# Kernel tuning notes

Measured on AMD Instinct MI355X. Metric: run time of the kernel, lower is better.

## Reference

```python
import jax, jax.numpy as jnp
import numpy as np

T, D, FF, E, K = 512, 2048, 768, 128, 8


def setup_inputs() -> dict:
    key = jax.random.key(0)
    k0, k1, k2, k3, k4 = jax.random.split(key, 5)
    scale = 0.02
    return {
        "hidden_states": jax.random.normal(k0, (T, D), dtype=jnp.float32),
        "w_gate": jax.random.normal(k1, (D, E), dtype=jnp.float32) * scale,  # router
        "w_gate_proj": jax.random.normal(k2, (E, D, FF), dtype=jnp.float32) * scale,
        "w_up_proj": jax.random.normal(k3, (E, D, FF), dtype=jnp.float32) * scale,
        "w_down_proj": jax.random.normal(k4, (E, FF, D), dtype=jnp.float32) * scale,
    }


def reference(hidden_states, w_gate, w_gate_proj, w_up_proj, w_down_proj):
    x = hidden_states  # [T, D]
    # Router: linear -> softmax (fp32) -> top-k -> renormalize (norm_topk_prob=True)
    router_logits = jnp.dot(x, w_gate)  # [T, E]
    probs = jax.nn.softmax(router_logits.astype(jnp.float32), axis=-1)
    topk_w, topk_idx = jax.lax.top_k(probs, K)  # [T, K]
    topk_w = topk_w / jnp.sum(topk_w, axis=-1, keepdims=True)
    topk_w = topk_w.astype(x.dtype)
    # Scatter per-(token,expert) combine weights: [T, E]
    rows = jnp.arange(T)[:, None]
    combine = jnp.zeros((T, E), dtype=x.dtype).at[rows, topk_idx].add(topk_w)
    # Grouped SwiGLU experts: scan over experts, weighted accumulation.
    def body(acc, per_expert):
        wg, wu, wd, s = per_expert  # [D,FF], [D,FF], [FF,D], [T]
        h = jax.nn.silu(jnp.dot(x, wg)) * jnp.dot(x, wu)  # [T, FF]
        return acc + s[:, None] * jnp.dot(h, wd), None

    init = jnp.zeros_like(x)
    out, _ = jax.lax.scan(
        body, init, (w_gate_proj, w_up_proj, w_down_proj, combine.T)
    )
    return out  # [T, D]
```

## Files before the change

### kernel.cpp

```cpp
#include <hip/hip_runtime.h>
#include <hip/hip_bf16.h>

#define TT 512
#define DH 2048
#define FFD 768
#define NE 128
#define TOPK 8
#define CAP 512
#define SMAX 64

typedef __attribute__((ext_vector_type(4))) float f32x4;
typedef __attribute__((ext_vector_type(8))) short short8;

typedef __attribute__((address_space(3))) unsigned int lds_u32_t;
typedef __attribute__((address_space(1))) unsigned int glob_u32_t;

__device__ __forceinline__ short f2bf(float f) {
    __hip_bfloat16 h = __float2bfloat16(f);
    return *reinterpret_cast<short*>(&h);
}

__device__ __forceinline__ void glds16(const float* g, float* l) {
    __builtin_amdgcn_global_load_lds((glob_u32_t*)g, (lds_u32_t*)l, 16, 0, 0);
}

#define VMCNT(N) asm volatile("s_waitcnt vmcnt(" #N ")" ::: "memory")

__global__ __launch_bounds__(256) void moe_init(int* __restrict__ cnt, float4* __restrict__ out)
{
    const int i = blockIdx.x * 256 + threadIdx.x;
    if (i < NE) cnt[i] = 0;
    out[i] = make_float4(0.f, 0.f, 0.f, 0.f);
}

__global__ __launch_bounds__(128) void moe_router(
    const float* __restrict__ x, const float* __restrict__ wg,
    int* __restrict__ cnt, int* __restrict__ tok_list, float* __restrict__ w_list)
{
    const int t = blockIdx.x;
    const int e = threadIdx.x;
    __shared__ float xs[DH];
    __shared__ float red[NE];
    __shared__ int   redi[NE];
    __shared__ float selw[TOPK];
    __shared__ int   seli[TOPK];

    for (int i = e; i < DH; i += 128) xs[i] = x[(size_t)t * DH + i];
    __syncthreads();

    float acc = 0.f;
    #pragma unroll 4
    for (int d = 0; d < DH; ++d)
        acc = fmaf(xs[d], wg[(size_t)d * NE + e], acc);

    red[e] = acc; __syncthreads();
    for (int s = 64; s > 0; s >>= 1) {
        if (e < s) red[e] = fmaxf(red[e], red[e + s]);
        __syncthreads();
    }
    const float mx = red[0];
    __syncthreads();

    float myp = __expf(acc - mx);

    for (int k = 0; k < TOPK; ++k) {
        red[e] = myp; redi[e] = e;
        __syncthreads();
        for (int s = 64; s > 0; s >>= 1) {
            if (e < s) {
                const float v2 = red[e + s]; const int i2 = redi[e + s];
                if (v2 > red[e] || (v2 == red[e] && i2 < redi[e])) { red[e] = v2; redi[e] = i2; }
            }
            __syncthreads();
        }
        if (e == 0) { selw[k] = red[0]; seli[k] = redi[0]; }
        __syncthreads();
        if (e == seli[k]) myp = -1.f;
        __syncthreads();
    }

    if (e == 0) {
        float s8 = 0.f;
        #pragma unroll
        for (int k = 0; k < TOPK; ++k) s8 += selw[k];
        const float inv = 1.f / s8;
        #pragma unroll
        for (int k = 0; k < TOPK; ++k) {
            const int ex = seli[k];
            const float wv = selw[k] * inv;
            const int pos = atomicAdd(&cnt[ex], 1);
            if (pos < CAP) {
                tok_list[ex * CAP + pos] = t * TOPK + k;
                w_list[ex * CAP + pos] = wv;
            }
        }
    }
}

__global__ __launch_bounds__(256) void moe_gather(
    const float* __restrict__ x, const int* __restrict__ cnt,
    const int* __restrict__ tok_list, short* __restrict__ xgb)
{
    const int e = blockIdx.x;
    int n = cnt[e]; if (n > SMAX) n = SMAX;
    const int k = threadIdx.x * 8;
    short* dste = xgb + (size_t)e * SMAX * DH;
    for (int s = 0; s < SMAX; ++s) {
        short8 o = {0, 0, 0, 0, 0, 0, 0, 0};
        if (s < n) {
            const float* xr = x + (size_t)(tok_list[e * CAP + s] >> 3) * DH + k;
            const float4 v0 = *(const float4*)(xr);
            const float4 v1 = *(const float4*)(xr + 4);
            o[0] = f2bf(v0.x); o[1] = f2bf(v0.y); o[2] = f2bf(v0.z); o[3] = f2bf(v0.w);
            o[4] = f2bf(v1.x); o[5] = f2bf(v1.y); o[6] = f2bf(v1.z); o[7] = f2bf(v1.w);
        }
        *(short8*)(dste + (size_t)s * DH + k) = o;
    }
}

__global__ __launch_bounds__(64) void moe_gateup(
    const short* __restrict__ xgb,
    const float* __restrict__ wgp, const float* __restrict__ wup,
    short* __restrict__ hc)
{
    __shared__ __align__(16) float Bsh[2 * 2 * 2048];

    const int e = blockIdx.y;
    const int lane = threadIdx.x;
    const int fl = lane & 15;
    const int g16 = lane >> 4;
    const int koff = g16 * 8;
    const int f0 = blockIdx.x * 64;
    const int lrow = lane >> 4;
    const int lcol = (lane & 15) * 4;

    const short* xge = xgb + (size_t)e * SMAX * DH;
    const float* wgs = wgp + (size_t)e * DH * FFD + f0;
    const float* wus = wup + (size_t)e * DH * FFD + f0;

    f32x4 accg[4][4] = {};
    f32x4 accu[4][4] = {};
    short8 aA[4], aB[4];

    auto ISSUE = [&](int kk, int b) {
        #pragma unroll
        for (int g = 0; g < 8; ++g) {
            const size_t ro = (size_t)(kk + g * 4 + lrow) * FFD + lcol;
            glds16(wgs + ro, &Bsh[b * 2048 + g * 256]);
            glds16(wus + ro, &Bsh[4096 + b * 2048 + g * 256]);
        }
    };
    auto LOADA = [&](int kk, short8 (&a)[4]) {
        #pragma unroll
        for (int fm = 0; fm < 4; ++fm)
            a[fm] = *(const short8*)(xge + (size_t)(fm * 16 + fl) * DH + kk + koff);
    };
    auto COMP = [&](int b, const short8 (&a)[4]) {
        #pragma unroll
        for (int nf = 0; nf < 4; ++nf) {
            const float* bg = &Bsh[b * 2048 + koff * 64 + nf * 16 + fl];
            const float* bu = &Bsh[4096 + b * 2048 + koff * 64 + nf * 16 + fl];
            short8 bfg, bfu;
            #pragma unroll
            for (int j = 0; j < 8; ++j) { bfg[j] = f2bf(bg[j * 64]); bfu[j] = f2bf(bu[j * 64]); }
            #pragma unroll
            for (int fm = 0; fm < 4; ++fm) {
                accg[nf][fm] = __builtin_amdgcn_mfma_f32_16x16x32_bf16(a[fm], bfg, accg[nf][fm], 0, 0, 0);
                accu[nf][fm] = __builtin_amdgcn_mfma_f32_16x16x32_bf16(a[fm], bfu, accu[nf][fm], 0, 0, 0);
            }
        }
    };

    ISSUE(0, 0);
    LOADA(0, aA);
    for (int t = 0; t < 63; ++t) {
        const int kk = (t + 1) * 32;
        ISSUE(kk, (t + 1) & 1);
        if (t & 1) LOADA(kk, aA); else LOADA(kk, aB);
        VMCNT(20);
        if (t & 1) COMP(1, aB); else COMP(0, aA);
    }
    VMCNT(0);
    COMP(1, aB);

    short* hce = hc + (size_t)e * SMAX * FFD + f0;
    #pragma unroll
    for (int nf = 0; nf < 4; ++nf) {
        #pragma unroll
        for (int fm = 0; fm < 4; ++fm) {
            #pragma unroll
            for (int r = 0; r < 4; ++r) {
                const int s = fm * 16 + g16 * 4 + r;
                const float g = accg[nf][fm][r];
                const float u = accu[nf][fm][r];
                const float hv = (g / (1.f + __expf(-g))) * u;
                hce[(size_t)s * FFD + nf * 16 + fl] = f2bf(hv);
            }
        }
    }
}

__global__ __launch_bounds__(64) void moe_down(
    const short* __restrict__ hc, const float* __restrict__ wdp,
    const int* __restrict__ cnt, const int* __restrict__ tok_list,
    const float* __restrict__ w_list, float* __restrict__ out)
{
    __shared__ __align__(16) float Bsh[2 * 2048];

    const int e = blockIdx.y;
    int n = cnt[e]; if (n > SMAX) n = SMAX;
    if (n == 0) return;

    const int lane = threadIdx.x;
    const int fl = lane & 15;
    const int g16 = lane >> 4;
    const int koff = g16 * 8;
    const int d0 = blockIdx.x * 64;
    const int lrow = lane >> 4;
    const int lcol = (lane & 15) * 4;

    const short* hce = hc + (size_t)e * SMAX * FFD;
    const float* wds = wdp + (size_t)e * FFD * DH + d0;

    f32x4 acc[4][4] = {};
    short8 aA[4], aB[4];

    auto ISSUE = [&](int kk, int b) {
        #pragma unroll
        for (int g = 0; g < 8; ++g) {
            const size_t ro = (size_t)(kk + g * 4 + lrow) * DH + lcol;
            glds16(wds + ro, &Bsh[b * 2048 + g * 256]);
        }
    };
    auto LOADA = [&](int kk, short8 (&a)[4]) {
        #pragma unroll
        for (int fm = 0; fm < 4; ++fm)
            a[fm] = *(const short8*)(hce + (size_t)(fm * 16 + fl) * FFD + kk + koff);
    };
    auto COMP = [&](int b, const short8 (&a)[4]) {
        #pragma unroll
        for (int nf = 0; nf < 4; ++nf) {
            const float* bp = &Bsh[b * 2048 + koff * 64 + nf * 16 + fl];
            short8 bf;
            #pragma unroll
            for (int j = 0; j < 8; ++j) bf[j] = f2bf(bp[j * 64]);
            #pragma unroll
            for (int fm = 0; fm < 4; ++fm)
                acc[nf][fm] = __builtin_amdgcn_mfma_f32_16x16x32_bf16(a[fm], bf, acc[nf][fm], 0, 0, 0);
        }
    };

    ISSUE(0, 0);
    LOADA(0, aA);
    for (int t = 0; t < 23; ++t) {
        const int kk = (t + 1) * 32;
        ISSUE(kk, (t + 1) & 1);
        if (t & 1) LOADA(kk, aA); else LOADA(kk, aB);
        VMCNT(12);
        if (t & 1) COMP(1, aB); else COMP(0, aA);
    }
    VMCNT(0);
    COMP(1, aB);

    #pragma unroll
    for (int nf = 0; nf < 4; ++nf) {
        #pragma unroll
        for (int fm = 0; fm < 4; ++fm) {
            #pragma unroll
            for (int r = 0; r < 4; ++r) {
                const int s = fm * 16 + g16 * 4 + r;
                if (s < n) {
                    const int t = tok_list[e * CAP + s] >> 3;
                    const float wt = w_list[e * CAP + s];
                    atomicAdd(out + (size_t)t * DH + d0 + nf * 16 + fl, acc[nf][fm][r] * wt);
                }
            }
        }
    }
}

extern "C" void kernel_launch(void* const* d_in, const int* in_sizes, int n_in,
                              void* d_out, int out_size, void* d_ws, size_t ws_size,
                              hipStream_t stream) {
    const float* x   = (const float*)d_in[0];
    const float* wg  = (const float*)d_in[1];
    const float* wgp = (const float*)d_in[2];
    const float* wup = (const float*)d_in[3];
    const float* wdp = (const float*)d_in[4];
    float* out = (float*)d_out;

    char* ws = (char*)d_ws;
    int*   cnt      = (int*)ws;
    int*   tok_list = (int*)(ws + 1024);
    float* w_list   = (float*)(ws + 1024 + NE * CAP * 4);
    short* xgb      = (short*)(ws + (1 << 20));
    short* hc       = (short*)(ws + (1 << 20) + (size_t)NE * SMAX * DH * 2);

    moe_init<<<1024, 256, 0, stream>>>(cnt, (float4*)out);
    moe_router<<<TT, 128, 0, stream>>>(x, wg, cnt, tok_list, w_list);
    moe_gather<<<NE, 256, 0, stream>>>(x, cnt, tok_list, xgb);
    moe_gateup<<<dim3(FFD / 64, NE), 64, 0, stream>>>(xgb, wgp, wup, hc);
    moe_down<<<dim3(DH / 64, NE), 64, 0, stream>>>(hc, wdp, cnt, tok_list, w_list, out);
}
```

Measured before the change: 813.8 us.

## Triple-buffer weight and activation prefetch in expert GEMMs; fold output zeroing into router

Both the gate/up and down expert kernels move from a double-buffered to a triple-buffered K-loop. Weight tiles stream into three LDS slots and activation fragments into three register sets, with two stages kept in flight and vmcnt waits sized to match. This should hide more global-memory latency while streaming the large fp32 expert weights. In exchange, LDS use per block rises (48 KB in gate/up), which may lower occupancy. Separately, zeroing of the output moves from the init kernel into the router kernel, leaving a tiny init that only clears the expert counters.

```diff
diff --git a/kernel.cpp b/kernel.cpp
--- a/kernel.cpp
+++ b/kernel.cpp
@@ -24,18 +24,20 @@
     __builtin_amdgcn_global_load_lds((glob_u32_t*)g, (lds_u32_t*)l, 16, 0, 0);
 }
 
-#define VMCNT(N) asm volatile("s_waitcnt vmcnt(" #N ")" ::: "memory")
-
-__global__ __launch_bounds__(256) void moe_init(int* __restrict__ cnt, float4* __restrict__ out)
-{
-    const int i = blockIdx.x * 256 + threadIdx.x;
-    if (i < NE) cnt[i] = 0;
-    out[i] = make_float4(0.f, 0.f, 0.f, 0.f);
+template<int N>
+__device__ __forceinline__ void vmwait() {
+    asm volatile("s_waitcnt vmcnt(%0)" :: "i"(N) : "memory");
+}
+
+__global__ __launch_bounds__(128) void moe_init(int* __restrict__ cnt)
+{
+    cnt[threadIdx.x] = 0;
 }
 
 __global__ __launch_bounds__(128) void moe_router(
     const float* __restrict__ x, const float* __restrict__ wg,
-    int* __restrict__ cnt, int* __restrict__ tok_list, float* __restrict__ w_list)
+    int* __restrict__ cnt, int* __restrict__ tok_list, float* __restrict__ w_list,
+    float* __restrict__ out)
 {
     const int t = blockIdx.x;
     const int e = threadIdx.x;
@@ -44,6 +46,11 @@
     __shared__ int   redi[NE];
     __shared__ float selw[TOPK];
     __shared__ int   seli[TOPK];
+
+    float4* outrow = (float4*)(out + (size_t)t * DH);
+    const float4 z4 = make_float4(0.f, 0.f, 0.f, 0.f);
+    #pragma unroll
+    for (int i = 0; i < 4; ++i) outrow[e + i * 128] = z4;
 
     for (int i = e; i < DH; i += 128) xs[i] = x[(size_t)t * DH + i];
     __syncthreads();
@@ -123,7 +130,7 @@
     const float* __restrict__ wgp, const float* __restrict__ wup,
     short* __restrict__ hc)
 {
-    __shared__ __align__(16) float Bsh[2 * 2 * 2048];
+    __shared__ __align__(16) float Bsh[6 * 2048];
 
     const int e = blockIdx.y;
     const int lane = threadIdx.x;
@@ -140,29 +147,36 @@
 
     f32x4 accg[4][4] = {};
     f32x4 accu[4][4] = {};
-    short8 aA[4], aB[4];
-
-    auto ISSUE = [&](int kk, int b) {
+    short8 A0[4], A1[4], A2[4];
+
+    auto ISSUE = [&](int t, int buf) {
+        const int kk = t * 32;
+        float* bg = &Bsh[buf * 2048];
+        float* bu = &Bsh[6144 + buf * 2048];
         #pragma unroll
         for (int g = 0; g < 8; ++g) {
             const size_t ro = (size_t)(kk + g * 4 + lrow) * FFD + lcol;
-            glds16(wgs + ro, &Bsh[b * 2048 + g * 256]);
-            glds16(wus + ro, &Bsh[4096 + b * 2048 + g * 256]);
-        }
-    };
-    auto LOADA = [&](int kk, short8 (&a)[4]) {
+            glds16(wgs + ro, bg + g * 256);
+            glds16(wus + ro, bu + g * 256);
+        }
+    };
+    auto LOADA = [&](int t, short8 (&a)[4]) {
+        const int kk = t * 32 + koff;
         #pragma unroll
         for (int fm = 0; fm < 4; ++fm)
-            a[fm] = *(const short8*)(xge + (size_t)(fm * 16 + fl) * DH + kk + koff);
-    };
-    auto COMP = [&](int b, const short8 (&a)[4]) {
+            a[fm] = *(const short8*)(xge + (size_t)(fm * 16 + fl) * DH + kk);
+    };
+    auto COMP = [&](int buf, const short8 (&a)[4]) {
+        const float* bg = &Bsh[buf * 2048 + koff * 64 + fl];
+        const float* bu = &Bsh[6144 + buf * 2048 + koff * 64 + fl];
         #pragma unroll
         for (int nf = 0; nf < 4; ++nf) {
-            const float* bg = &Bsh[b * 2048 + koff * 64 + nf * 16 + fl];
-            const float* bu = &Bsh[4096 + b * 2048 + koff * 64 + nf * 16 + fl];
             short8 bfg, bfu;
             #pragma unroll
-            for (int j = 0; j < 8; ++j) { bfg[j] = f2bf(bg[j * 64]); bfu[j] = f2bf(bu[j * 64]); }
+            for (int j = 0; j < 8; ++j) {
+                bfg[j] = f2bf(bg[nf * 16 + j * 64]);
+                bfu[j] = f2bf(bu[nf * 16 + j * 64]);
+            }
             #pragma unroll
             for (int fm = 0; fm < 4; ++fm) {
                 accg[nf][fm] = __builtin_amdgcn_mfma_f32_16x16x32_bf16(a[fm], bfg, accg[nf][fm], 0, 0, 0);
@@ -171,17 +185,18 @@
         }
     };
 
-    ISSUE(0, 0);
-    LOADA(0, aA);
-    for (int t = 0; t < 63; ++t) {
-        const int kk = (t + 1) * 32;
-        ISSUE(kk, (t + 1) & 1);
-        if (t & 1) LOADA(kk, aA); else LOADA(kk, aB);
-        VMCNT(20);
-        if (t & 1) COMP(1, aB); else COMP(0, aA);
-    }
-    VMCNT(0);
-    COMP(1, aB);
+    LOADA(0, A0); ISSUE(0, 0);
+    LOADA(1, A1); ISSUE(1, 1);
+    for (int i = 0; i < 20; ++i) {
+        const int t = 3 * i;
+        LOADA(t + 2, A2); ISSUE(t + 2, 2); vmwait<40>(); COMP(0, A0);
+        LOADA(t + 3, A0); ISSUE(t + 3, 0); vmwait<40>(); COMP(1, A1);
+        LOADA(t + 4, A1); ISSUE(t + 4, 1); vmwait<40>(); COMP(2, A2);
+    }
+    LOADA(62, A2); ISSUE(62, 2); vmwait<40>(); COMP(0, A0);
+    LOADA(63, A0); ISSUE(63, 0); vmwait<40>(); COMP(1, A1);
+    vmwait<20>(); COMP(2, A2);
+    vmwait<0>();  COMP(0, A0);
 
     short* hce = hc + (size_t)e * SMAX * FFD + f0;
     #pragma unroll
@@ -205,7 +220,7 @@
     const int* __restrict__ cnt, const int* __restrict__ tok_list,
     const float* __restrict__ w_list, float* __restrict__ out)
 {
-    __shared__ __align__(16) float Bsh[2 * 2048];
+    __shared__ __align__(16) float Bsh[3 * 2048];
 
     const int e = blockIdx.y;
     int n = cnt[e]; if (n > SMAX) n = SMAX;
@@ -223,44 +238,50 @@
     const float* wds = wdp + (size_t)e * FFD * DH + d0;
 
     f32x4 acc[4][4] = {};
-    short8 aA[4], aB[4];
-
-    auto ISSUE = [&](int kk, int b) {
+    short8 A0[4], A1[4], A2[4];
+
+    auto ISSUE = [&](int t, int buf) {
+        const int kk = t * 32;
+        float* bd = &Bsh[buf * 2048];
         #pragma unroll
         for (int g = 0; g < 8; ++g) {
             const size_t ro = (size_t)(kk + g * 4 + lrow) * DH + lcol;
-            glds16(wds + ro, &Bsh[b * 2048 + g * 256]);
-        }
-    };
-    auto LOADA = [&](int kk, short8 (&a)[4]) {
+            glds16(wds + ro, bd + g * 256);
+        }
+    };
+    auto LOADA = [&](int t, short8 (&a)[4]) {
+        const int kk = t * 32 + koff;
         #pragma unroll
         for (int fm = 0; fm < 4; ++fm)
-            a[fm] = *(const short8*)(hce + (size_t)(fm * 16 + fl) * FFD + kk + koff);
-    };
-    auto COMP = [&](int b, const short8 (&a)[4]) {
+            a[fm] = *(const short8*)(hce + (size_t)(fm * 16 + fl) * FFD + kk);
+    };
+    auto COMP = [&](int buf, const short8 (&a)[4]) {
+        const float* bp = &Bsh[buf * 2048 + koff * 64 + fl];
         #pragma unroll
         for (int nf = 0; nf < 4; ++nf) {
-            const float* bp = &Bsh[b * 2048 + koff * 64 + nf * 16 + fl];
             short8 bf;
             #pragma unroll
-            for (int j = 0; j < 8; ++j) bf[j] = f2bf(bp[j * 64]);
+            for (int j = 0; j < 8; ++j) bf[j] = f2bf(bp[nf * 16 + j * 64]);
             #pragma unroll
             for (int fm = 0; fm < 4; ++fm)
                 acc[nf][fm] = __builtin_amdgcn_mfma_f32_16x16x32_bf16(a[fm], bf, acc[nf][fm], 0, 0, 0);
         }
     };
 
-    ISSUE(0, 0);
-    LOADA(0, aA);
-    for (int t = 0; t < 23; ++t) {
-        const int kk = (t + 1) * 32;
-        ISSUE(kk, (t + 1) & 1);
-        if (t & 1) LOADA(kk, aA); else LOADA(kk, aB);
-        VMCNT(12);
-        if (t & 1) COMP(1, aB); else COMP(0, aA);
-    }
-    VMCNT(0);
-    COMP(1, aB);
+    LOADA(0, A0); ISSUE(0, 0);
+    LOADA(1, A1); ISSUE(1, 1);
+    for (int i = 0; i < 6; ++i) {
+        const int t = 3 * i;
+        LOADA(t + 2, A2); ISSUE(t + 2, 2); vmwait<24>(); COMP(0, A0);
+        LOADA(t + 3, A0); ISSUE(t + 3, 0); vmwait<24>(); COMP(1, A1);
+        LOADA(t + 4, A1); ISSUE(t + 4, 1); vmwait<24>(); COMP(2, A2);
+    }
+    LOADA(20, A2); ISSUE(20, 2); vmwait<24>(); COMP(0, A0);
+    LOADA(21, A0); ISSUE(21, 0); vmwait<24>(); COMP(1, A1);
+    LOADA(22, A1); ISSUE(22, 1); vmwait<24>(); COMP(2, A2);
+    LOADA(23, A2); ISSUE(23, 2); vmwait<24>(); COMP(0, A0);
+    vmwait<12>(); COMP(1, A1);
+    vmwait<0>();  COMP(2, A2);
 
     #pragma unroll
     for (int nf = 0; nf < 4; ++nf) {
@@ -296,8 +317,8 @@
     short* xgb      = (short*)(ws + (1 << 20));
     short* hc       = (short*)(ws + (1 << 20) + (size_t)NE * SMAX * DH * 2);
 
-    moe_init<<<1024, 256, 0, stream>>>(cnt, (float4*)out);
-    moe_router<<<TT, 128, 0, stream>>>(x, wg, cnt, tok_list, w_list);
+    moe_init<<<1, 128, 0, stream>>>(cnt);
+    moe_router<<<TT, 128, 0, stream>>>(x, wg, cnt, tok_list, w_list, out);
     moe_gather<<<NE, 256, 0, stream>>>(x, cnt, tok_list, xgb);
     moe_gateup<<<dim3(FFD / 64, NE), 64, 0, stream>>>(xgb, wgp, wup, hc);
     moe_down<<<dim3(DH / 64, NE), 64, 0, stream>>>(hc, wdp, cnt, tok_list, w_list, out);
```

Result: faster. 777.1 us (-4.5%).
